# Performance work log

Hardware: AMD Instinct MI355X
Metric: run time of the kernel (lower is better)

Reference implementation:

```python
import jax, jax.numpy as jnp
import numpy as np

NUM_STEPS = 5  # DVF2DDF(num_steps=5)


def _warp(vol, ddf, mode):
    """MONAI Warp: sample vol at (voxel index + ddf), align_corners=True, zeros padding.
    vol: [N,C,D,H,W]; ddf: [N,3,D,H,W] (channels = d,h,w displacement)."""
    N, C, D, H, W = vol.shape
    gd, gh, gw = jnp.meshgrid(jnp.arange(D, dtype=ddf.dtype),
                              jnp.arange(H, dtype=ddf.dtype),
                              jnp.arange(W, dtype=ddf.dtype), indexing='ij')
    cd = gd + ddf[:, 0]  # [N,D,H,W] absolute sample coords
    ch = gh + ddf[:, 1]
    cw = gw + ddf[:, 2]
    vol_flat = vol.reshape(N, C, D * H * W)

    def gather(di, hi, wi, valid):
        dc = jnp.clip(di, 0, D - 1)
        hc = jnp.clip(hi, 0, H - 1)
        wc = jnp.clip(wi, 0, W - 1)
        flat = ((dc * H + hc) * W + wc).reshape(N, 1, -1)
        v = jnp.take_along_axis(vol_flat, flat, axis=2).reshape(N, C, D, H, W)
        return v * valid[:, None]

    def in_bounds(di, hi, wi):
        return ((di >= 0) & (di < D) & (hi >= 0) & (hi < H)
                & (wi >= 0) & (wi < W)).astype(vol.dtype)

    if mode == 'nearest':
        di = jnp.round(cd).astype(jnp.int32)
        hi = jnp.round(ch).astype(jnp.int32)
        wi = jnp.round(cw).astype(jnp.int32)
        return gather(di, hi, wi, in_bounds(di, hi, wi))

    # trilinear ('bilinear' in grid_sample naming)
    d0 = jnp.floor(cd); h0 = jnp.floor(ch); w0 = jnp.floor(cw)
    fd = cd - d0; fh = ch - h0; fw = cw - w0
    d0i = d0.astype(jnp.int32); h0i = h0.astype(jnp.int32); w0i = w0.astype(jnp.int32)
    out = jnp.zeros_like(vol)
    for dd in (0, 1):
        for dh in (0, 1):
            for dw in (0, 1):
                di = d0i + dd; hi = h0i + dh; wi = w0i + dw
                wgt = ((fd if dd else 1 - fd)
                       * (fh if dh else 1 - fh)
                       * (fw if dw else 1 - fw))
                out = out + gather(di, hi, wi, in_bounds(di, hi, wi)) * wgt[:, None]
    return out


def _dvf2ddf(dvf, num_steps=NUM_STEPS):
    """Scaling-and-squaring integration of a stationary velocity field (MONAI DVF2DDF)."""
    ddf = dvf / (2 ** num_steps)
    for _ in range(num_steps):
        ddf = ddf + _warp(ddf, ddf, 'bilinear')
    return ddf


def setup_inputs() -> dict:
    key = jax.random.key(0)
    ks = jax.random.split(key, 6)
    D = H = W = 160
    return {
        "dvf0": jax.random.normal(ks[0], (1, 3, D, H, W), jnp.float32),
        "dvf1": jax.random.normal(ks[1], (1, 3, D, H, W), jnp.float32),
        "image": jax.random.normal(ks[2], (1, 1, D, H, W), jnp.float32),
        "cavity": jax.random.randint(ks[3], (1, 1, D, H, W), 0, 5, jnp.int32),
        "coronary": jax.random.randint(ks[4], (1, 1, D, H, W), 0, 3, jnp.int32),
        "w": jax.random.uniform(ks[5], (), jnp.float32),
    }


def reference(dvf0, dvf1, image, cavity, coronary, w):
    # linear blend of the two neighbouring phase DVFs
    dvf = dvf0 * (1 - w) + dvf1 * w
    ddf = _dvf2ddf(dvf)
    img_warped = _warp(image, ddf, 'bilinear')
    # labels are concatenated along batch and warped with nearest, ddf repeated
    labels = jnp.concatenate([cavity, coronary], axis=0).astype(jnp.float32)  # [2,1,D,H,W]
    lab_warped = _warp(labels, jnp.tile(ddf, (2, 1, 1, 1, 1)), 'nearest')
    cav_warped = lab_warped[0][None].astype(jnp.uint8)
    cor_warped = lab_warped[1][None].astype(jnp.uint8)
    return img_warped, cav_warped, cor_warped, ddf
```

## Files before the change

kernel.cpp:

```cpp
#include <hip/hip_runtime.h>

#define DD 160
#define HH 160
#define WW 160
#define PL (HH*WW)
#define S (DD*PL)

__device__ __forceinline__ float fmul(float a, float b){ return __fmul_rn(a,b); }
__device__ __forceinline__ float fadd(float a, float b){ return __fadd_rn(a,b); }
__device__ __forceinline__ float fsub(float a, float b){ return __fsub_rn(a,b); }


template<int H>
__global__ __launch_bounds__(256) void warp_step(const float* __restrict__ in,
                                                 float* __restrict__ out) {
    constexpr int RZ = 4 + 2 * H;
    constexpr int RY = 8 + 2 * H;
    constexpr int ROWS = RZ * RY;
    constexpr int NCH4 = ROWS * 10;
    constexpr int CHF  = ROWS * 40;
    __shared__ float smem[3 * CHF];

    int b  = (blockIdx.x & 7) * 500 + (blockIdx.x >> 3);
    int ix = b % 5;
    int r  = b / 5;
    int iy = r % 20;
    int iz = r / 20;
    int x0 = ix << 5, y0 = iy << 3, z0 = iz << 2;
    int xs4 = x0 - 4, ys = y0 - H, zs = z0 - H;

    int tid = threadIdx.x;
    for (int c = tid; c < NCH4; c += 256) {
        int row = c / 10;
        int col = (c - row * 10) << 2;
        int rz  = row / RY;
        int ry  = row - rz * RY;
        int cz = min(max(zs + rz, 0), DD - 1);
        int cy = min(max(ys + ry, 0), HH - 1);
        int q  = min(max((cz * HH + cy) * WW + xs4 + col, 0), S - 4);
        float4 v0 = *(const float4*)(in + q);
        float4 v1 = *(const float4*)(in + S + q);
        float4 v2 = *(const float4*)(in + 2 * S + q);
        *(float4*)&smem[row * 40 + col]           = v0;
        *(float4*)&smem[CHF + row * 40 + col]     = v1;
        *(float4*)&smem[2 * CHF + row * 40 + col] = v2;
    }
    __syncthreads();

    int lane = tid & 63, wid = tid >> 6;
    int x = x0 | (lane & 31);
    int y = y0 | (wid << 1) | (lane >> 5);
    int lx = x - xs4;
    int ly = y - ys;

    for (int j = 0; j < 4; ++j) {
        int z = z0 + j;
        int p = (z * HH + y) * WW + x;
        int lc = ((j + H) * RY + ly) * 40 + lx;
        float vd = smem[lc], vh = smem[CHF + lc], vw = smem[2 * CHF + lc];

        float cd = fadd((float)z, vd);
        float ch = fadd((float)y, vh);
        float cw = fadd((float)x, vw);

        float d0 = floorf(cd), h0 = floorf(ch), w0 = floorf(cw);
        float fd = fsub(cd, d0), fh = fsub(ch, h0), fw = fsub(cw, w0);
        float gd = fsub(1.0f, fd), gh = fsub(1.0f, fh), gw = fsub(1.0f, fw);
        int d0i = (int)d0, h0i = (int)h0, w0i = (int)w0;

        int rd = d0i - zs, rh = h0i - ys, rw = w0i - xs4;
        bool ok = ((unsigned)rd < (unsigned)(RZ - 1))
                & ((unsigned)rh < (unsigned)(RY - 1))
                & ((unsigned)rw < 39u);

        float r0, r1, r2;
        if (ok) {
            bool vA0 = (d0i >= 0), vA1 = (d0i + 1 < DD);
            bool vB0 = (h0i >= 0), vB1 = (h0i + 1 < HH);
            bool vC0 = (w0i >= 0), vC1 = (w0i + 1 < WW);
            float wt[8];
            #pragma unroll
            for (int t = 0; t < 8; ++t) {
                int dd = t >> 2, dh = (t >> 1) & 1, dw = t & 1;
                bool valid = (dd ? vA1 : vA0) & (dh ? vB1 : vB0) & (dw ? vC1 : vC0);
                float wgt = fmul(fmul(dd ? fd : gd, dh ? fh : gh), dw ? fw : gw);
                wt[t] = valid ? wgt : 0.0f;
            }
            int l0 = (rd * RY + rh) * 40 + rw;
            const int off[8] = { 0, 1, 40, 41,
                                 RY * 40, RY * 40 + 1, (RY + 1) * 40, (RY + 1) * 40 + 1 };
            float acc0 = 0.0f, acc1 = 0.0f, acc2 = 0.0f;
            #pragma unroll
            for (int t = 0; t < 8; ++t) {
                int li = l0 + off[t];
                acc0 = fadd(acc0, fmul(smem[li], wt[t]));
                acc1 = fadd(acc1, fmul(smem[CHF + li], wt[t]));
                acc2 = fadd(acc2, fmul(smem[2 * CHF + li], wt[t]));
            }
            r0 = fadd(vd, acc0);
            r1 = fadd(vh, acc1);
            r2 = fadd(vw, acc2);
        } else {
            int   qa[8];
            float wt[8];
            #pragma unroll
            for (int t = 0; t < 8; ++t) {
                int dd = t >> 2, dh = (t >> 1) & 1, dw = t & 1;
                int di = d0i + dd, hi = h0i + dh, wi = w0i + dw;
                bool valid = (di >= 0) & (di < DD) & (hi >= 0) & (hi < HH)
                           & (wi >= 0) & (wi < WW);
                float wgt = fmul(fmul(dd ? fd : gd, dh ? fh : gh), dw ? fw : gw);
                wt[t] = valid ? wgt : 0.0f;
                int dc = min(max(di, 0), DD - 1);
                int hc = min(max(hi, 0), HH - 1);
                int wc = min(max(wi, 0), WW - 1);
                qa[t] = (dc * HH + hc) * WW + wc;
            }
            float acc0 = 0.0f, acc1 = 0.0f, acc2 = 0.0f;
            #pragma unroll
            for (int t = 0; t < 8; ++t) {
                acc0 = fadd(acc0, fmul(in[qa[t]], wt[t]));
                acc1 = fadd(acc1, fmul(in[S + qa[t]], wt[t]));
                acc2 = fadd(acc2, fmul(in[2 * S + qa[t]], wt[t]));
            }
            r0 = fadd(vd, acc0);
            r1 = fadd(vh, acc1);
            r2 = fadd(vw, acc2);
        }

        out[p] = r0; out[S + p] = r1; out[2 * S + p] = r2;
    }
}

__global__ __launch_bounds__(256) void fused_init_s1(const float* __restrict__ dvf0,
                                                     const float* __restrict__ dvf1,
                                                     const float* __restrict__ wp,
                                                     float* __restrict__ out) {
    constexpr int H = 1, RZ = 6, RY = 10, ROWS = 60, NCH4 = 600, CHF = 2400;
    __shared__ float smem[3 * CHF];
    float w = wp[0];
    float onew = fsub(1.0f, w);

    int b  = (blockIdx.x & 7) * 500 + (blockIdx.x >> 3);
    int ix = b % 5;
    int r  = b / 5;
    int iy = r % 20;
    int iz = r / 20;
    int x0 = ix << 5, y0 = iy << 3, z0 = iz << 2;
    int xs4 = x0 - 4, ys = y0 - H, zs = z0 - H;

    int tid = threadIdx.x;
    for (int c = tid; c < NCH4; c += 256) {
        int row = c / 10;
        int col = (c - row * 10) << 2;
        int rz  = row / RY;
        int ry  = row - rz * RY;
        int cz = min(max(zs + rz, 0), DD - 1);
        int cy = min(max(ys + ry, 0), HH - 1);
        int q  = min(max((cz * HH + cy) * WW + xs4 + col, 0), S - 4);
        #pragma unroll
        for (int ch = 0; ch < 3; ++ch) {
            float A[4], B[4], O[4];
            *(float4*)A = *(const float4*)(dvf0 + (size_t)ch * S + q);
            *(float4*)B = *(const float4*)(dvf1 + (size_t)ch * S + q);
            #pragma unroll
            for (int k = 0; k < 4; ++k)
                O[k] = fmul(fadd(fmul(A[k], onew), fmul(B[k], w)), 0.03125f);
            *(float4*)&smem[ch * CHF + row * 40 + col] = *(float4*)O;
        }
    }
    __syncthreads();

    int lane = tid & 63, wid = tid >> 6;
    int x = x0 | (lane & 31);
    int y = y0 | (wid << 1) | (lane >> 5);
    int lx = x - xs4;
    int ly = y - ys;

    for (int j = 0; j < 4; ++j) {
        int z = z0 + j;
        int p = (z * HH + y) * WW + x;
        int lc = ((j + H) * RY + ly) * 40 + lx;
        float vd = smem[lc], vh = smem[CHF + lc], vw = smem[2 * CHF + lc];

        float cd = fadd((float)z, vd);
        float ch = fadd((float)y, vh);
        float cw = fadd((float)x, vw);

        float d0 = floorf(cd), h0 = floorf(ch), w0 = floorf(cw);
        float fd = fsub(cd, d0), fh = fsub(ch, h0), fw = fsub(cw, w0);
        float gd = fsub(1.0f, fd), gh = fsub(1.0f, fh), gw = fsub(1.0f, fw);
        int d0i = (int)d0, h0i = (int)h0, w0i = (int)w0;

        int rd = d0i - zs, rh = h0i - ys, rw = w0i - xs4;
        bool ok = ((unsigned)rd < (unsigned)(RZ - 1))
                & ((unsigned)rh < (unsigned)(RY - 1))
                & ((unsigned)rw < 39u);

        float r0, r1, r2;
        if (ok) {
            bool vA0 = (d0i >= 0), vA1 = (d0i + 1 < DD);
            bool vB0 = (h0i >= 0), vB1 = (h0i + 1 < HH);
            bool vC0 = (w0i >= 0), vC1 = (w0i + 1 < WW);
            float wt[8];
            #pragma unroll
            for (int t = 0; t < 8; ++t) {
                int dd = t >> 2, dh = (t >> 1) & 1, dw = t & 1;
                bool valid = (dd ? vA1 : vA0) & (dh ? vB1 : vB0) & (dw ? vC1 : vC0);
                float wgt = fmul(fmul(dd ? fd : gd, dh ? fh : gh), dw ? fw : gw);
                wt[t] = valid ? wgt : 0.0f;
            }
            int l0 = (rd * RY + rh) * 40 + rw;
            const int off[8] = { 0, 1, 40, 41,
                                 RY * 40, RY * 40 + 1, (RY + 1) * 40, (RY + 1) * 40 + 1 };
            float acc0 = 0.0f, acc1 = 0.0f, acc2 = 0.0f;
            #pragma unroll
            for (int t = 0; t < 8; ++t) {
                int li = l0 + off[t];
                acc0 = fadd(acc0, fmul(smem[li], wt[t]));
                acc1 = fadd(acc1, fmul(smem[CHF + li], wt[t]));
                acc2 = fadd(acc2, fmul(smem[2 * CHF + li], wt[t]));
            }
            r0 = fadd(vd, acc0);
            r1 = fadd(vh, acc1);
            r2 = fadd(vw, acc2);
        } else {
            int   qa[8];
            float wt[8];
            #pragma unroll
            for (int t = 0; t < 8; ++t) {
                int dd = t >> 2, dh = (t >> 1) & 1, dw = t & 1;
                int di = d0i + dd, hi = h0i + dh, wi = w0i + dw;
                bool valid = (di >= 0) & (di < DD) & (hi >= 0) & (hi < HH)
                           & (wi >= 0) & (wi < WW);
                float wgt = fmul(fmul(dd ? fd : gd, dh ? fh : gh), dw ? fw : gw);
                wt[t] = valid ? wgt : 0.0f;
                int dc = min(max(di, 0), DD - 1);
                int hc = min(max(hi, 0), HH - 1);
                int wc = min(max(wi, 0), WW - 1);
                qa[t] = (dc * HH + hc) * WW + wc;
            }
            float acc0 = 0.0f, acc1 = 0.0f, acc2 = 0.0f;
            #pragma unroll
            for (int t = 0; t < 8; ++t) {
                float ga = fmul(fadd(fmul(dvf0[qa[t]], onew), fmul(dvf1[qa[t]], w)), 0.03125f);
                float gb = fmul(fadd(fmul(dvf0[S + qa[t]], onew), fmul(dvf1[S + qa[t]], w)), 0.03125f);
                float gc = fmul(fadd(fmul(dvf0[2 * S + qa[t]], onew), fmul(dvf1[2 * S + qa[t]], w)), 0.03125f);
                acc0 = fadd(acc0, fmul(ga, wt[t]));
                acc1 = fadd(acc1, fmul(gb, wt[t]));
                acc2 = fadd(acc2, fmul(gc, wt[t]));
            }
            r0 = fadd(vd, acc0);
            r1 = fadd(vh, acc1);
            r2 = fadd(vw, acc2);
        }

        out[p] = r0; out[S + p] = r1; out[2 * S + p] = r2;
    }
}

__global__ __launch_bounds__(256) void final_phased(const float* __restrict__ ddf4,
                                                    const float* __restrict__ image,
                                                    const int* __restrict__ cav,
                                                    const int* __restrict__ cor,
                                                    float* __restrict__ outImg,
                                                    float* __restrict__ outDdf) {
    constexpr int RZ = 10, RY = 14, ROWS = 140, NCH4 = 1400, CHF = 5600;
    __shared__ float smem[CHF];

    int b  = (blockIdx.x & 7) * 500 + (blockIdx.x >> 3);
    int ix = b % 5;
    int r  = b / 5;
    int iy = r % 20;
    int iz = r / 20;
    int x0 = ix << 5, y0 = iy << 3, z0 = iz << 2;
    int xs4 = x0 - 4, ys = y0 - 3, zs = z0 - 3;

    int tid = threadIdx.x;
    int lane = tid & 63, wid = tid >> 6;
    int x = x0 | (lane & 31);
    int y = y0 | (wid << 1) | (lane >> 5);
    int p0 = (z0 * HH + y) * WW + x;

    float ctd[4], cth[4], ctw[4];
    #pragma unroll
    for (int j = 0; j < 4; ++j) {
        ctd[j] = ddf4[p0 + j * PL];
        cth[j] = ddf4[S + p0 + j * PL];
        ctw[j] = ddf4[2 * S + p0 + j * PL];
    }

    float wt[4][8];
    int   l0[4];
    int   okm = 0;
    const int off[8] = { 0, 1, 40, 41,
                         RY * 40, RY * 40 + 1, (RY + 1) * 40, (RY + 1) * 40 + 1 };
    #pragma unroll
    for (int j = 0; j < 4; ++j) {
        int z = z0 + j;
        float cd = fadd((float)z, ctd[j]);
        float ch = fadd((float)y, cth[j]);
        float cw = fadd((float)x, ctw[j]);
        float d0 = floorf(cd), h0 = floorf(ch), w0 = floorf(cw);
        float fd = fsub(cd, d0), fh = fsub(ch, h0), fw = fsub(cw, w0);
        float gd = fsub(1.0f, fd), gh = fsub(1.0f, fh), gw = fsub(1.0f, fw);
        int d0i = (int)d0, h0i = (int)h0, w0i = (int)w0;

        bool vA0 = (d0i >= 0), vA1 = (d0i + 1 < DD);
        bool vB0 = (h0i >= 0), vB1 = (h0i + 1 < HH);
        bool vC0 = (w0i >= 0), vC1 = (w0i + 1 < WW);
        #pragma unroll
        for (int t = 0; t < 8; ++t) {
            int dd = t >> 2, dh = (t >> 1) & 1, dw = t & 1;
            bool valid = (dd ? vA1 : vA0) & (dh ? vB1 : vB0) & (dw ? vC1 : vC0);
            float wgt = fmul(fmul(dd ? fd : gd, dh ? fh : gh), dw ? fw : gw);
            wt[j][t] = valid ? wgt : 0.0f;
        }
        int rd = d0i - zs, rh = h0i - ys, rw = w0i - xs4;
        bool ok = ((unsigned)rd < (unsigned)(RZ - 1))
                & ((unsigned)rh < (unsigned)(RY - 1))
                & ((unsigned)rw < 39u);
        l0[j] = (rd * RY + rh) * 40 + rw;
        okm |= (ok ? 1 : 0) << j;
    }

    float acc[3][4] = {{0,0,0,0},{0,0,0,0},{0,0,0,0}};
    #pragma unroll
    for (int c = 0; c < 3; ++c) {
        if (c) __syncthreads();
        const float* src = ddf4 + (size_t)c * S;
        for (int cc = tid; cc < NCH4; cc += 256) {
            int row = cc / 10;
            int col = (cc - row * 10) << 2;
            int rz  = row / RY;
            int ry  = row - rz * RY;
            int cz = min(max(zs + rz, 0), DD - 1);
            int cy = min(max(ys + ry, 0), HH - 1);
            int q  = min(max((cz * HH + cy) * WW + xs4 + col, 0), S - 4);
            *(float4*)&smem[row * 40 + col] = *(const float4*)(src + q);
        }
        __syncthreads();
        #pragma unroll
        for (int j = 0; j < 4; ++j) {
            if ((okm >> j) & 1) {
                #pragma unroll
                for (int t = 0; t < 8; ++t)
                    acc[c][j] = fadd(acc[c][j], fmul(smem[l0[j] + off[t]], wt[j][t]));
            }
        }
    }

    #pragma unroll
    for (int j = 0; j < 4; ++j) {
        int z = z0 + j;
        int p = p0 + j * PL;
        float r0, r1, r2;
        if ((okm >> j) & 1) {
            r0 = fadd(ctd[j], acc[0][j]);
            r1 = fadd(cth[j], acc[1][j]);
            r2 = fadd(ctw[j], acc[2][j]);
        } else {
            float cd = fadd((float)z, ctd[j]);
            float ch = fadd((float)y, cth[j]);
            float cw = fadd((float)x, ctw[j]);
            float d0 = floorf(cd), h0 = floorf(ch), w0 = floorf(cw);
            float fd = fsub(cd, d0), fh = fsub(ch, h0), fw = fsub(cw, w0);
            float gd = fsub(1.0f, fd), gh = fsub(1.0f, fh), gw = fsub(1.0f, fw);
            int d0i = (int)d0, h0i = (int)h0, w0i = (int)w0;
            int   qa[8];
            float wtf[8];
            #pragma unroll
            for (int t = 0; t < 8; ++t) {
                int dd = t >> 2, dh = (t >> 1) & 1, dw = t & 1;
                int di = d0i + dd, hi = h0i + dh, wi = w0i + dw;
                bool valid = (di >= 0) & (di < DD) & (hi >= 0) & (hi < HH)
                           & (wi >= 0) & (wi < WW);
                float wgt = fmul(fmul(dd ? fd : gd, dh ? fh : gh), dw ? fw : gw);
                wtf[t] = valid ? wgt : 0.0f;
                int dc = min(max(di, 0), DD - 1);
                int hc = min(max(hi, 0), HH - 1);
                int wc = min(max(wi, 0), WW - 1);
                qa[t] = (dc * HH + hc) * WW + wc;
            }
            float a0 = 0.0f, a1 = 0.0f, a2 = 0.0f;
            #pragma unroll
            for (int t = 0; t < 8; ++t) {
                a0 = fadd(a0, fmul(ddf4[qa[t]], wtf[t]));
                a1 = fadd(a1, fmul(ddf4[S + qa[t]], wtf[t]));
                a2 = fadd(a2, fmul(ddf4[2 * S + qa[t]], wtf[t]));
            }
            r0 = fadd(ctd[j], a0);
            r1 = fadd(cth[j], a1);
            r2 = fadd(ctw[j], a2);
        }
        outDdf[p] = r0; outDdf[S + p] = r1; outDdf[2 * S + p] = r2;

        float cd2 = fadd((float)z, r0);
        float ch2 = fadd((float)y, r1);
        float cw2 = fadd((float)x, r2);
        float d02 = floorf(cd2), h02 = floorf(ch2), w02 = floorf(cw2);
        float fd2 = fsub(cd2, d02), fh2 = fsub(ch2, h02), fw2 = fsub(cw2, w02);
        float gd2 = fsub(1.0f, fd2), gh2 = fsub(1.0f, fh2), gw2 = fsub(1.0f, fw2);
        int d2i = (int)d02, h2i = (int)h02, w2i = (int)w02;

        bool fast = ((unsigned)d2i < (unsigned)(DD - 1))
                  & ((unsigned)h2i < (unsigned)(HH - 1))
                  & ((unsigned)w2i < (unsigned)(WW - 1));
        if (fast) {
            const float* bp0 = image + (d2i * HH + h2i) * WW + w2i;
            const float* bp1 = bp0 + PL;
            float g[8];
            g[0] = bp0[0];      g[1] = bp0[1];
            g[2] = bp0[WW];     g[3] = bp0[WW + 1];
            g[4] = bp1[0];      g[5] = bp1[1];
            g[6] = bp1[WW];     g[7] = bp1[WW + 1];
            float w00 = fmul(gd2, gh2), w01 = fmul(gd2, fh2);
            float w10 = fmul(fd2, gh2), w11 = fmul(fd2, fh2);
            float wtf[8] = { fmul(w00, gw2), fmul(w00, fw2), fmul(w01, gw2), fmul(w01, fw2),
                             fmul(w10, gw2), fmul(w10, fw2), fmul(w11, gw2), fmul(w11, fw2) };
            float a = 0.0f;
            #pragma unroll
            for (int t = 0; t < 8; ++t) a = fadd(a, fmul(g[t], wtf[t]));
            outImg[p] = a;

            int di = (int)rintf(cd2), hi = (int)rintf(ch2), wi = (int)rintf(cw2);
            int q = (di * HH + hi) * WW + wi;
            outImg[S + p]     = (float)cav[q];
            outImg[2 * S + p] = (float)cor[q];
        } else {
            int   qb[8];
            float wtf[8];
            #pragma unroll
            for (int t = 0; t < 8; ++t) {
                int dd = t >> 2, dh = (t >> 1) & 1, dw = t & 1;
                int di = d2i + dd, hi = h2i + dh, wi = w2i + dw;
                bool valid = (di >= 0) & (di < DD) & (hi >= 0) & (hi < HH)
                           & (wi >= 0) & (wi < WW);
                float wgt = fmul(fmul(dd ? fd2 : gd2, dh ? fh2 : gh2), dw ? fw2 : gw2);
                wtf[t] = valid ? wgt : 0.0f;
                int dc = min(max(di, 0), DD - 1);
                int hc = min(max(hi, 0), HH - 1);
                int wc = min(max(wi, 0), WW - 1);
                qb[t] = (dc * HH + hc) * WW + wc;
            }
            float a = 0.0f;
            #pragma unroll
            for (int t = 0; t < 8; ++t) a = fadd(a, fmul(image[qb[t]], wtf[t]));
            outImg[p] = a;

            int di = (int)rintf(cd2), hi = (int)rintf(ch2), wi = (int)rintf(cw2);
            bool valid = (di >= 0) & (di < DD) & (hi >= 0) & (hi < HH)
                       & (wi >= 0) & (wi < WW);
            int dc = min(max(di, 0), DD - 1);
            int hc = min(max(hi, 0), HH - 1);
            int wc = min(max(wi, 0), WW - 1);
            int q = (dc * HH + hc) * WW + wc;
            outImg[S + p]     = valid ? (float)cav[q] : 0.0f;
            outImg[2 * S + p] = valid ? (float)cor[q] : 0.0f;
        }
    }
}

__global__ __launch_bounds__(256) void warp_flat(const float* __restrict__ in,
                                                 float* __restrict__ out) {
    int b  = (blockIdx.x & 7) * 1000 + (blockIdx.x >> 3);
    int ix = b % 5;
    int r  = b / 5;
    int iy = r % 20;
    int iz = r / 20;
    int lane = threadIdx.x & 63, wid = threadIdx.x >> 6;
    int x  = (ix << 5) | (lane & 31);
    int y  = (iy << 3) | (wid << 1) | (lane >> 5);
    int z0 = iz << 1;
    int p0 = (z0 * HH + y) * WW + x;

    #pragma unroll
    for (int j = 0; j < 2; ++j) {
        int z = z0 + j;
        int p = p0 + j * PL;
        float vd = in[p], vh = in[S + p], vw = in[2 * S + p];
        float cd = fadd((float)z, vd);
        float ch = fadd((float)y, vh);
        float cw = fadd((float)x, vw);

        float d0 = floorf(cd), h0 = floorf(ch), w0 = floorf(cw);
        float fd = fsub(cd, d0), fh = fsub(ch, h0), fw = fsub(cw, w0);
        float gd = fsub(1.0f, fd), gh = fsub(1.0f, fh), gw = fsub(1.0f, fw);
        int d0i = (int)d0, h0i = (int)h0, w0i = (int)w0;

        int   qa[8];
        float wt[8];
        #pragma unroll
        for (int t = 0; t < 8; ++t) {
            int dd = t >> 2, dh = (t >> 1) & 1, dw = t & 1;
            int di = d0i + dd, hi = h0i + dh, wi = w0i + dw;
            bool valid = (di >= 0) & (di < DD) & (hi >= 0) & (hi < HH)
                       & (wi >= 0) & (wi < WW);
            float wgt = fmul(fmul(dd ? fd : gd, dh ? fh : gh), dw ? fw : gw);
            wt[t] = valid ? wgt : 0.0f;
            int dc = min(max(di, 0), DD - 1);
            int hc = min(max(hi, 0), HH - 1);
            int wc = min(max(wi, 0), WW - 1);
            qa[t] = (dc * HH + hc) * WW + wc;
        }
        float acc0 = 0.0f, acc1 = 0.0f, acc2 = 0.0f;
        #pragma unroll
        for (int t = 0; t < 8; ++t) {
            acc0 = fadd(acc0, fmul(in[qa[t]], wt[t]));
            acc1 = fadd(acc1, fmul(in[S + qa[t]], wt[t]));
            acc2 = fadd(acc2, fmul(in[2 * S + qa[t]], wt[t]));
        }
        out[p]         = fadd(vd, acc0);
        out[S + p]     = fadd(vh, acc1);
        out[2 * S + p] = fadd(vw, acc2);
    }
}

__global__ __launch_bounds__(256) void final_kernel(const float* __restrict__ ddf,
                                                    const float* __restrict__ image,
                                                    const int* __restrict__ cav,
                                                    const int* __restrict__ cor,
                                                    float* __restrict__ out) {
    int b  = (blockIdx.x & 7) * 1000 + (blockIdx.x >> 3);
    int ix = b % 5;
    int r  = b / 5;
    int iy = r % 20;
    int iz = r / 20;
    int lane = threadIdx.x & 63, wid = threadIdx.x >> 6;
    int x  = (ix << 5) | (lane & 31);
    int y  = (iy << 3) | (wid << 1) | (lane >> 5);
    int z0 = iz << 1;
    int p0 = (z0 * HH + y) * WW + x;

    #pragma unroll
    for (int j = 0; j < 2; ++j) {
        int z = z0 + j;
        int p = p0 + j * PL;
        float cd = fadd((float)z, ddf[p]);
        float ch = fadd((float)y, ddf[S + p]);
        float cw = fadd((float)x, ddf[2 * S + p]);

        float d0 = floorf(cd), h0 = floorf(ch), w0 = floorf(cw);
        float fd = fsub(cd, d0), fh = fsub(ch, h0), fw = fsub(cw, w0);
        float gd = fsub(1.0f, fd), gh = fsub(1.0f, fh), gw = fsub(1.0f, fw);
        int d0i = (int)d0, h0i = (int)h0, w0i = (int)w0;

        int   qa[8];
        float wt[8];
        #pragma unroll
        for (int t = 0; t < 8; ++t) {
            int dd = t >> 2, dh = (t >> 1) & 1, dw = t & 1;
            int di = d0i + dd, hi = h0i + dh, wi = w0i + dw;
            bool valid = (di >= 0) & (di < DD) & (hi >= 0) & (hi < HH)
                       & (wi >= 0) & (wi < WW);
            float wgt = fmul(fmul(dd ? fd : gd, dh ? fh : gh), dw ? fw : gw);
            wt[t] = valid ? wgt : 0.0f;
            int dc = min(max(di, 0), DD - 1);
            int hc = min(max(hi, 0), HH - 1);
            int wc = min(max(wi, 0), WW - 1);
            qa[t] = (dc * HH + hc) * WW + wc;
        }
        float acc = 0.0f;
        #pragma unroll
        for (int t = 0; t < 8; ++t) acc = fadd(acc, fmul(image[qa[t]], wt[t]));
        out[p] = acc;

        int di = (int)rintf(cd), hi = (int)rintf(ch), wi = (int)rintf(cw);
        bool valid = (di >= 0) & (di < DD) & (hi >= 0) & (hi < HH)
                   & (wi >= 0) & (wi < WW);
        int dc = min(max(di, 0), DD - 1);
        int hc = min(max(hi, 0), HH - 1);
        int wc = min(max(wi, 0), WW - 1);
        int q = (dc * HH + hc) * WW + wc;
        out[S + p]     = valid ? (float)cav[q] : 0.0f;
        out[2 * S + p] = valid ? (float)cor[q] : 0.0f;
    }
}

extern "C" void kernel_launch(void* const* d_in, const int* in_sizes, int n_in,
                              void* d_out, int out_size, void* d_ws, size_t ws_size,
                              hipStream_t stream) {
    const float* dvf0   = (const float*)d_in[0];
    const float* dvf1   = (const float*)d_in[1];
    const float* image  = (const float*)d_in[2];
    const int*   cav    = (const int*)d_in[3];
    const int*   cor    = (const int*)d_in[4];
    const float* w      = (const float*)d_in[5];

    float* out  = (float*)d_out;
    float* bufA = out;
    float* bufB = out + (size_t)3 * S;
    float* bufC = (float*)d_ws;
    bool useWs = (d_ws != nullptr) && (ws_size >= (size_t)3 * S * sizeof(float));

    fused_init_s1<<<4000, 256, 0, stream>>>(dvf0, dvf1, w, bufB);
    warp_step<1><<<4000, 256, 0, stream>>>(bufB, bufA);
    warp_step<1><<<4000, 256, 0, stream>>>(bufA, bufB);
    if (useWs) {
        warp_step<2><<<4000, 256, 0, stream>>>(bufB, bufC);
        final_phased<<<4000, 256, 0, stream>>>(bufC, image, cav, cor, bufA, bufB);
    } else {
        warp_step<2><<<4000, 256, 0, stream>>>(bufB, bufA);
        warp_flat<<<8000, 256, 0, stream>>>(bufA, bufB);
        final_kernel<<<8000, 256, 0, stream>>>(bufB, image, cav, cor, bufA);
    }
}
```

Before: 376.8 us.

## Use direct global-to-LDS loads and double-buffer channel tiles in final kernel

Replaces the register-staged float4 halo loads with global_load_lds builtins that write straight into shared memory in the warp_step kernel and the final kernel. In the final kernel, the shared buffer is doubled so the next displacement channel's tile is fetched while the current one is interpolated, and the first channel's fetch is issued before the centre loads and weight setup. The out-of-tile fallback gathers are moved ahead of the barrier so they overlap the DMA. This costs twice the LDS in the final kernel, which may lower occupancy, and relies on the async LDS load completing by the time of the __syncthreads barrier.

```diff
diff --git a/kernel.cpp b/kernel.cpp
--- a/kernel.cpp
+++ b/kernel.cpp
@@ -9,6 +9,13 @@
 __device__ __forceinline__ float fmul(float a, float b){ return __fmul_rn(a,b); }
 __device__ __forceinline__ float fadd(float a, float b){ return __fadd_rn(a,b); }
 __device__ __forceinline__ float fsub(float a, float b){ return __fsub_rn(a,b); }
+
+__device__ __forceinline__ void dma16(const float* g, float* l) {
+    __builtin_amdgcn_global_load_lds(
+        (const __attribute__((address_space(1))) unsigned int*)g,
+        (__attribute__((address_space(3))) unsigned int*)l,
+        16, 0, 0);
+}
 
 
 template<int H>
@@ -19,7 +26,7 @@
     constexpr int ROWS = RZ * RY;
     constexpr int NCH4 = ROWS * 10;
     constexpr int CHF  = ROWS * 40;
-    __shared__ float smem[3 * CHF];
+    __shared__ __align__(16) float smem[3 * CHF];
 
     int b  = (blockIdx.x & 7) * 500 + (blockIdx.x >> 3);
     int ix = b % 5;
@@ -38,12 +45,9 @@
         int cz = min(max(zs + rz, 0), DD - 1);
         int cy = min(max(ys + ry, 0), HH - 1);
         int q  = min(max((cz * HH + cy) * WW + xs4 + col, 0), S - 4);
-        float4 v0 = *(const float4*)(in + q);
-        float4 v1 = *(const float4*)(in + S + q);
-        float4 v2 = *(const float4*)(in + 2 * S + q);
-        *(float4*)&smem[row * 40 + col]           = v0;
-        *(float4*)&smem[CHF + row * 40 + col]     = v1;
-        *(float4*)&smem[2 * CHF + row * 40 + col] = v2;
+        dma16(in + q,         smem + (c << 2));
+        dma16(in + S + q,     smem + CHF + (c << 2));
+        dma16(in + 2 * S + q, smem + 2 * CHF + (c << 2));
     }
     __syncthreads();
 
@@ -137,7 +141,7 @@
                                                      const float* __restrict__ wp,
                                                      float* __restrict__ out) {
     constexpr int H = 1, RZ = 6, RY = 10, ROWS = 60, NCH4 = 600, CHF = 2400;
-    __shared__ float smem[3 * CHF];
+    __shared__ __align__(16) float smem[3 * CHF];
     float w = wp[0];
     float onew = fsub(1.0f, w);
 
@@ -266,7 +270,7 @@
                                                     float* __restrict__ outImg,
                                                     float* __restrict__ outDdf) {
     constexpr int RZ = 10, RY = 14, ROWS = 140, NCH4 = 1400, CHF = 5600;
-    __shared__ float smem[CHF];
+    __shared__ __align__(16) float smem[2 * CHF];
 
     int b  = (blockIdx.x & 7) * 500 + (blockIdx.x >> 3);
     int ix = b % 5;
@@ -281,6 +285,18 @@
     int x = x0 | (lane & 31);
     int y = y0 | (wid << 1) | (lane >> 5);
     int p0 = (z0 * HH + y) * WW + x;
+
+    #pragma unroll 1
+    for (int cc = tid; cc < NCH4; cc += 256) {
+        int row = cc / 10;
+        int col = (cc - row * 10) << 2;
+        int rz  = row / RY;
+        int ry  = row - rz * RY;
+        int cz = min(max(zs + rz, 0), DD - 1);
+        int cy = min(max(ys + ry, 0), HH - 1);
+        int q  = min(max((cz * HH + cy) * WW + xs4 + col, 0), S - 4);
+        dma16(ddf4 + q, smem + (cc << 2));
+    }
 
     float ctd[4], cth[4], ctw[4];
     #pragma unroll
@@ -324,76 +340,92 @@
         okm |= (ok ? 1 : 0) << j;
     }
 
-    float acc[3][4] = {{0,0,0,0},{0,0,0,0},{0,0,0,0}};
+    float fb[3][4];
+    if (okm != 15) {
+        #pragma unroll
+        for (int j = 0; j < 4; ++j) {
+            if (!((okm >> j) & 1)) {
+                int z = z0 + j;
+                float cd = fadd((float)z, ctd[j]);
+                float ch = fadd((float)y, cth[j]);
+                float cw = fadd((float)x, ctw[j]);
+                float d0 = floorf(cd), h0 = floorf(ch), w0 = floorf(cw);
+                float fd = fsub(cd, d0), fh = fsub(ch, h0), fw = fsub(cw, w0);
+                float gd = fsub(1.0f, fd), gh = fsub(1.0f, fh), gw = fsub(1.0f, fw);
+                int d0i = (int)d0, h0i = (int)h0, w0i = (int)w0;
+                int   qa[8];
+                float wtf[8];
+                #pragma unroll
+                for (int t = 0; t < 8; ++t) {
+                    int dd = t >> 2, dh = (t >> 1) & 1, dw = t & 1;
+                    int di = d0i + dd, hi = h0i + dh, wi = w0i + dw;
+                    bool valid = (di >= 0) & (di < DD) & (hi >= 0) & (hi < HH)
+                               & (wi >= 0) & (wi < WW);
+                    float wgt = fmul(fmul(dd ? fd : gd, dh ? fh : gh), dw ? fw : gw);
+                    wtf[t] = valid ? wgt : 0.0f;
+                    int dc = min(max(di, 0), DD - 1);
+                    int hc = min(max(hi, 0), HH - 1);
+                    int wc = min(max(wi, 0), WW - 1);
+                    qa[t] = (dc * HH + hc) * WW + wc;
+                }
+                float a0 = 0.0f, a1 = 0.0f, a2 = 0.0f;
+                #pragma unroll
+                for (int t = 0; t < 8; ++t) {
+                    a0 = fadd(a0, fmul(ddf4[qa[t]], wtf[t]));
+                    a1 = fadd(a1, fmul(ddf4[S + qa[t]], wtf[t]));
+                    a2 = fadd(a2, fmul(ddf4[2 * S + qa[t]], wtf[t]));
+                }
+                fb[0][j] = a0; fb[1][j] = a1; fb[2][j] = a2;
+            }
+        }
+    }
+
+    __syncthreads();
+
+    float rr[3][4];
     #pragma unroll
     for (int c = 0; c < 3; ++c) {
-        if (c) __syncthreads();
-        const float* src = ddf4 + (size_t)c * S;
-        for (int cc = tid; cc < NCH4; cc += 256) {
-            int row = cc / 10;
-            int col = (cc - row * 10) << 2;
-            int rz  = row / RY;
-            int ry  = row - rz * RY;
-            int cz = min(max(zs + rz, 0), DD - 1);
-            int cy = min(max(ys + ry, 0), HH - 1);
-            int q  = min(max((cz * HH + cy) * WW + xs4 + col, 0), S - 4);
-            *(float4*)&smem[row * 40 + col] = *(const float4*)(src + q);
-        }
-        __syncthreads();
+        if (c < 2) {
+            const float* src = ddf4 + (size_t)(c + 1) * S;
+            float* buf = smem + ((c + 1) & 1) * CHF;
+            #pragma unroll 1
+            for (int cc = tid; cc < NCH4; cc += 256) {
+                int row = cc / 10;
+                int col = (cc - row * 10) << 2;
+                int rz  = row / RY;
+                int ry  = row - rz * RY;
+                int cz = min(max(zs + rz, 0), DD - 1);
+                int cy = min(max(ys + ry, 0), HH - 1);
+                int q  = min(max((cz * HH + cy) * WW + xs4 + col, 0), S - 4);
+                dma16(src + q, buf + (cc << 2));
+            }
+        }
+        const float* g = smem + (c & 1) * CHF;
+        float ctr_c = 0.0f;
         #pragma unroll
         for (int j = 0; j < 4; ++j) {
+            float acc = 0.0f;
             if ((okm >> j) & 1) {
                 #pragma unroll
                 for (int t = 0; t < 8; ++t)
-                    acc[c][j] = fadd(acc[c][j], fmul(smem[l0[j] + off[t]], wt[j][t]));
-            }
-        }
+                    acc = fadd(acc, fmul(g[l0[j] + off[t]], wt[j][t]));
+                float ctr = (c == 0) ? ctd[j] : (c == 1) ? cth[j] : ctw[j];
+                rr[c][j] = fadd(ctr, acc);
+            } else {
+                float ctr = (c == 0) ? ctd[j] : (c == 1) ? cth[j] : ctw[j];
+                rr[c][j] = fadd(ctr, fb[c][j]);
+            }
+            outDdf[(size_t)c * S + p0 + j * PL] = rr[c][j];
+        }
+        (void)ctr_c;
+        __syncthreads();
     }
 
     #pragma unroll
     for (int j = 0; j < 4; ++j) {
         int z = z0 + j;
         int p = p0 + j * PL;
-        float r0, r1, r2;
-        if ((okm >> j) & 1) {
-            r0 = fadd(ctd[j], acc[0][j]);
-            r1 = fadd(cth[j], acc[1][j]);
-            r2 = fadd(ctw[j], acc[2][j]);
-        } else {
-            float cd = fadd((float)z, ctd[j]);
-            float ch = fadd((float)y, cth[j]);
-            float cw = fadd((float)x, ctw[j]);
-            float d0 = floorf(cd), h0 = floorf(ch), w0 = floorf(cw);
-            float fd = fsub(cd, d0), fh = fsub(ch, h0), fw = fsub(cw, w0);
-            float gd = fsub(1.0f, fd), gh = fsub(1.0f, fh), gw = fsub(1.0f, fw);
-            int d0i = (int)d0, h0i = (int)h0, w0i = (int)w0;
-            int   qa[8];
-            float wtf[8];
-            #pragma unroll
-            for (int t = 0; t < 8; ++t) {
-                int dd = t >> 2, dh = (t >> 1) & 1, dw = t & 1;
-                int di = d0i + dd, hi = h0i + dh, wi = w0i + dw;
-                bool valid = (di >= 0) & (di < DD) & (hi >= 0) & (hi < HH)
-                           & (wi >= 0) & (wi < WW);
-                float wgt = fmul(fmul(dd ? fd : gd, dh ? fh : gh), dw ? fw : gw);
-                wtf[t] = valid ? wgt : 0.0f;
-                int dc = min(max(di, 0), DD - 1);
-                int hc = min(max(hi, 0), HH - 1);
-                int wc = min(max(wi, 0), WW - 1);
-                qa[t] = (dc * HH + hc) * WW + wc;
-            }
-            float a0 = 0.0f, a1 = 0.0f, a2 = 0.0f;
-            #pragma unroll
-            for (int t = 0; t < 8; ++t) {
-                a0 = fadd(a0, fmul(ddf4[qa[t]], wtf[t]));
-                a1 = fadd(a1, fmul(ddf4[S + qa[t]], wtf[t]));
-                a2 = fadd(a2, fmul(ddf4[2 * S + qa[t]], wtf[t]));
-            }
-            r0 = fadd(ctd[j], a0);
-            r1 = fadd(cth[j], a1);
-            r2 = fadd(ctw[j], a2);
-        }
-        outDdf[p] = r0; outDdf[S + p] = r1; outDdf[2 * S + p] = r2;
+        float r0 = rr[0][j], r1 = rr[1][j], r2 = rr[2][j];
 
         float cd2 = fadd((float)z, r0);
         float ch2 = fadd((float)y, r1);
```

Result: faster. 366.5 us (-2.7%).
